# Optimization experiments

Hardware: AMD Instinct MI355X
Metric: run time of the kernel (lower is better)

Reference implementation:

```python
import jax, jax.numpy as jnp
import numpy as np

NUM_HEADS = 16


def setup_inputs() -> dict:
    key = jax.random.key(0)
    ks = jax.random.split(key, 5)
    B, L, D = 2, 2048, 1024
    x = jax.random.normal(ks[0], (B, L, D), dtype=jnp.float32)
    s = 1.0 / np.sqrt(D)
    Wqkv_w = jax.random.normal(ks[1], (3 * D, D), dtype=jnp.float32) * s
    Wqkv_b = jax.random.normal(ks[2], (3 * D,), dtype=jnp.float32) * 0.01
    out_w = jax.random.normal(ks[3], (D, D), dtype=jnp.float32) * s
    out_b = jax.random.normal(ks[4], (D,), dtype=jnp.float32) * 0.01
    return {"x": x, "Wqkv_w": Wqkv_w, "Wqkv_b": Wqkv_b, "out_w": out_w, "out_b": out_b}


def reference(x, Wqkv_w, Wqkv_b, out_w, out_b):
    B, L, D = x.shape
    H = NUM_HEADS
    d = D // H
    scale = 1.0 / np.sqrt(d).astype(np.float32)
    # qkv projection: torch Linear is x @ W^T + b
    qkv = x @ Wqkv_w.T + Wqkv_b                      # [B, L, 3D]
    qkv = qkv.reshape(B, L, 3, H, d)                 # (three h d) split
    qkv = jnp.transpose(qkv, (2, 0, 3, 1, 4))        # [3, B, H, L, d]
    q, k, v = qkv[0], qkv[1], qkv[2]
    k = k * scale
    # Linear-attention recurrence S_t = S_{t-1} + v_t k_t^T, y_t = S_t q_t
    # == causally-masked unnormalized attention: y_t = sum_{s<=t} (q_t.k_s) v_s
    scores = jnp.einsum('bhld,bhmd->bhlm', q, k)     # [B,H,L,L]
    causal = jnp.tril(jnp.ones((L, L), dtype=scores.dtype))
    y = jnp.einsum('bhlm,bhmd->bhld', scores * causal, v)  # [B,H,L,d]
    y = jnp.transpose(y, (0, 2, 1, 3)).reshape(B, L, D)    # b l (h d)
    return y @ out_w.T + out_b
```

## Files before the change

### kernel.cpp

```cpp
#include <hip/hip_runtime.h>


#define DEV __device__ __forceinline__

typedef __attribute__((ext_vector_type(8))) short bf16x8;
typedef __attribute__((ext_vector_type(4))) float f32x4;

DEV ushort f2bf(float f) {
  union { float f; unsigned u; } v; v.f = f;
  unsigned r = v.u + 0x7fffu + ((v.u >> 16) & 1u);
  return (ushort)(r >> 16);
}
DEV float bf2f(unsigned b) {
  union { unsigned u; float f; } v; v.u = (b & 0xffffu) << 16;
  return v.f;
}
DEV void glds16(const ushort* g, ushort* l) {
  __builtin_amdgcn_global_load_lds(
      (const __attribute__((address_space(1))) unsigned int*)g,
      (__attribute__((address_space(3))) unsigned int*)l, 16, 0, 0);
}

__global__ __launch_bounds__(256) void cvt_all(const float* __restrict__ x,
                                               const float* __restrict__ Ww,
                                               const float* __restrict__ Ow,
                                               ushort* __restrict__ xb,
                                               ushort* __restrict__ wqkvb,
                                               ushort* __restrict__ outwb) {
  int i = blockIdx.x * 256 + threadIdx.x;
  const float* src; ushort* dst; int off;
  if (i < 1048576)      { src = x;  dst = xb;    off = i; }
  else if (i < 1835008) { src = Ww; dst = wqkvb; off = i - 1048576; }
  else                  { src = Ow; dst = outwb; off = i - 1835008; }
  float4 v = ((const float4*)src)[off];
  ushort4 o;
  o.x = f2bf(v.x); o.y = f2bf(v.y); o.z = f2bf(v.z); o.w = f2bf(v.w);
  ((ushort4*)dst)[off] = o;
}

template <bool OUT_BF16, bool KSCALE>
__global__ __launch_bounds__(256) void gemm_bt(const ushort* __restrict__ A,
                                               const ushort* __restrict__ Bw,
                                               const float* __restrict__ bias,
                                               void* __restrict__ Cout,
                                               int M, int N, int K) {
  __shared__ ushort As[128 * 32];
  __shared__ ushort Bs[128 * 32];
  const int t = threadIdx.x;
  const int wid = t >> 6, lane = t & 63;
  const int quad = lane >> 4, l16 = lane & 15;
  const int bm = blockIdx.y * 128, bn = blockIdx.x * 128;
  const int wm = (wid >> 1) * 64, wn = (wid & 1) * 64;

  f32x4 acc[4][4];
  const f32x4 z = {0.f, 0.f, 0.f, 0.f};
#pragma unroll
  for (int i = 0; i < 4; ++i)
#pragma unroll
    for (int j = 0; j < 4; ++j) acc[i][j] = z;

  const ushort* ag = A + (size_t)(bm + (t >> 2)) * K + ((t & 3) * 8);
  const ushort* bg = Bw + (size_t)(bn + (t >> 2)) * K + ((t & 3) * 8);
  ushort* asl = As + wid * 512;
  ushort* bsl = Bs + wid * 512;
  const size_t rowskip = (size_t)64 * K;

  for (int k0 = 0; k0 < K; k0 += 32) {
    glds16(ag + k0, asl);
    glds16(ag + k0 + rowskip, asl + 2048);
    glds16(bg + k0, bsl);
    glds16(bg + k0 + rowskip, bsl + 2048);
    __syncthreads();
    bf16x8 af[4], bf[4];
#pragma unroll
    for (int i = 0; i < 4; ++i) {
      af[i] = *(const bf16x8*)(As + (wm + i * 16 + l16) * 32 + quad * 8);
      bf[i] = *(const bf16x8*)(Bs + (wn + i * 16 + l16) * 32 + quad * 8);
    }
#pragma unroll
    for (int i = 0; i < 4; ++i)
#pragma unroll
      for (int j = 0; j < 4; ++j)
        acc[i][j] = __builtin_amdgcn_mfma_f32_16x16x32_bf16(af[i], bf[j], acc[i][j], 0, 0, 0);
    __syncthreads();
  }

#pragma unroll
  for (int i = 0; i < 4; ++i)
#pragma unroll
    for (int j = 0; j < 4; ++j) {
      const int col = bn + wn + j * 16 + l16;
      const float bv = bias[col];
      float sc = 1.f;
      if (KSCALE) sc = ((col >> 10) == 1) ? 0.125f : 1.f;
#pragma unroll
      for (int r = 0; r < 4; ++r) {
        const int row = bm + wm + i * 16 + quad * 4 + r;
        const float v = (acc[i][j][r] + bv) * sc;
        if (OUT_BF16)
          ((ushort*)Cout)[(size_t)row * N + col] = f2bf(v);
        else
          ((float*)Cout)[(size_t)row * N + col] = v;
      }
    }
}

__global__ __launch_bounds__(256) void gemm_out64(const ushort* __restrict__ A,
                                                  const ushort* __restrict__ Bw,
                                                  const float* __restrict__ bias,
                                                  float* __restrict__ C,
                                                  int M, int N, int K) {
  __shared__ ushort As[64 * 32];
  __shared__ ushort Bs[128 * 32];
  const int t = threadIdx.x;
  const int wid = t >> 6, lane = t & 63;
  const int quad = lane >> 4, l16 = lane & 15;
  const int bm = blockIdx.y * 64, bn = blockIdx.x * 128;
  const int wn = wid * 32;

  f32x4 acc[4][2];
  const f32x4 z = {0.f, 0.f, 0.f, 0.f};
#pragma unroll
  for (int i = 0; i < 4; ++i) { acc[i][0] = z; acc[i][1] = z; }

  const ushort* ag = A + (size_t)(bm + (t >> 2)) * K + ((t & 3) * 8);
  const ushort* bg = Bw + (size_t)(bn + (t >> 2)) * K + ((t & 3) * 8);
  ushort* asl = As + wid * 512;
  ushort* bsl = Bs + wid * 512;
  const size_t rowskip = (size_t)64 * K;

  for (int k0 = 0; k0 < K; k0 += 32) {
    glds16(ag + k0, asl);
    glds16(bg + k0, bsl);
    glds16(bg + k0 + rowskip, bsl + 2048);
    __syncthreads();
    bf16x8 af[4], bf[2];
#pragma unroll
    for (int i = 0; i < 4; ++i)
      af[i] = *(const bf16x8*)(As + (i * 16 + l16) * 32 + quad * 8);
#pragma unroll
    for (int j = 0; j < 2; ++j)
      bf[j] = *(const bf16x8*)(Bs + (wn + j * 16 + l16) * 32 + quad * 8);
#pragma unroll
    for (int i = 0; i < 4; ++i)
#pragma unroll
      for (int j = 0; j < 2; ++j)
        acc[i][j] = __builtin_amdgcn_mfma_f32_16x16x32_bf16(af[i], bf[j], acc[i][j], 0, 0, 0);
    __syncthreads();
  }

#pragma unroll
  for (int i = 0; i < 4; ++i)
#pragma unroll
    for (int j = 0; j < 2; ++j) {
      const int col = bn + wn + j * 16 + l16;
      const float bv = bias[col];
#pragma unroll
      for (int r = 0; r < 4; ++r) {
        const int row = bm + i * 16 + quad * 4 + r;
        C[(size_t)row * N + col] = acc[i][j][r] + bv;
      }
    }
}

__global__ __launch_bounds__(256) void kv_local(const ushort* __restrict__ qkv,
                                                float* __restrict__ mlocT) {
  const int c = blockIdx.x, bh = blockIdx.y;
  const int b = bh >> 4, hd = bh & 15;
  const int t = threadIdx.x;
  const int wid = t >> 6, lane = t & 63;
  const int quad = lane >> 4, l16 = lane & 15;
  __shared__ ushort kT[64 * 136];
  __shared__ ushort vT[64 * 136];

  {
    const int row = t & 127;
    const int isv = t >> 7;
    const ushort* g = qkv + (size_t)(b * 2048 + c * 128 + row) * 3072 +
                      1024 + isv * 1024 + hd * 64;
    ushort tmp[64];
#pragma unroll
    for (int q = 0; q < 8; ++q) *(uint4*)(tmp + q * 8) = *(const uint4*)(g + q * 8);
    ushort* dst = isv ? vT : kT;
#pragma unroll
    for (int j = 0; j < 64; ++j) dst[j * 136 + row] = tmp[j];
  }
  __syncthreads();

  const f32x4 z = {0.f, 0.f, 0.f, 0.f};
  f32x4 acc[4];
#pragma unroll
  for (int ct = 0; ct < 4; ++ct) acc[ct] = z;
#pragma unroll
  for (int kc = 0; kc < 4; ++kc) {
    bf16x8 afr = *(const bf16x8*)(vT + (wid * 16 + l16) * 136 + kc * 32 + quad * 8);
#pragma unroll
    for (int ct = 0; ct < 4; ++ct) {
      bf16x8 bfr = *(const bf16x8*)(kT + (ct * 16 + l16) * 136 + kc * 32 + quad * 8);
      acc[ct] = __builtin_amdgcn_mfma_f32_16x16x32_bf16(afr, bfr, acc[ct], 0, 0, 0);
    }
  }

  float* outp = mlocT + ((size_t)bh * 16 + c) * 4096;
#pragma unroll
  for (int ct = 0; ct < 4; ++ct)
#pragma unroll
    for (int r = 0; r < 4; ++r)
      outp[(wid * 16 + quad * 4 + r) * 64 + ct * 16 + l16] = acc[ct][r];
}

__global__ __launch_bounds__(256) void attn_chunk(const ushort* __restrict__ qkv,
                                                  const float* __restrict__ mlocT,
                                                  ushort* __restrict__ yb) {
  const int c = blockIdx.x, bh = blockIdx.y;
  const int b = bh >> 4, hd = bh & 15;
  const int l0 = c * 128;
  const int t = threadIdx.x;
  const int wid = t >> 6, lane = t & 63;
  const int quad = lane >> 4, l16 = lane & 15;

  __shared__ ushort P[16384];
  __shared__ ushort U[16384];
  ushort* Qs = U;
  ushort* Ks = U + 8192;
  ushort* vT = U;
  ushort* sT = U + 8704;

  {
    uint4 zz; zz.x = zz.y = zz.z = zz.w = 0u;
    uint4* p4 = (uint4*)P;
#pragma unroll
    for (int i = 0; i < 8; ++i) p4[i * 256 + t] = zz;
  }
  {
    const int kcs = ((lane & 7) ^ (lane >> 3)) * 8;
    const ushort* qg = qkv + (size_t)(b * 2048 + l0 + (t >> 3)) * 3072 + hd * 64 + kcs;
    ushort* ql = Qs + wid * 512;
    ushort* kl = Ks + wid * 512;
#pragma unroll
    for (int h2 = 0; h2 < 4; ++h2) {
      glds16(qg + (size_t)h2 * 32 * 3072, ql + h2 * 2048);
      glds16(qg + (size_t)h2 * 32 * 3072 + 1024, kl + h2 * 2048);
    }
  }

  float run[16];
#pragma unroll
  for (int j = 0; j < 16; ++j) run[j] = 0.f;
  {
    const float4* mb = (const float4*)mlocT + (size_t)bh * 16384 + (size_t)t * 4;
    for (int cp = 0; cp < c; ++cp) {
      const float4* mc = mb + (size_t)cp * 1024;
#pragma unroll
      for (int k = 0; k < 4; ++k) {
        const float4 m = mc[k];
        run[k * 4 + 0] += m.x; run[k * 4 + 1] += m.y;
        run[k * 4 + 2] += m.z; run[k * 4 + 3] += m.w;
      }
    }
  }
  __syncthreads();

  bf16x8 qf[2][2];
#pragma unroll
  for (int i = 0; i < 2; ++i)
#pragma unroll
    for (int kc = 0; kc < 2; ++kc)
      qf[i][kc] = *(const bf16x8*)(Qs + ((wid * 2 + i) * 16 + l16) * 64 +
                                   (((kc * 4 + quad) ^ (l16 & 7)) * 8));

  const f32x4 z4 = {0.f, 0.f, 0.f, 0.f};
  f32x4 pacc[2][8];
#pragma unroll
  for (int i = 0; i < 2; ++i)
#pragma unroll
    for (int j = 0; j < 8; ++j) pacc[i][j] = z4;

#pragma unroll
  for (int i = 0; i < 2; ++i) {
    const int rt = wid * 2 + i;
#pragma unroll
    for (int tj = 0; tj < 8; ++tj) {
      if (tj <= rt) {
#pragma unroll
        for (int kc = 0; kc < 2; ++kc) {
          bf16x8 kfr = *(const bf16x8*)(Ks + (tj * 16 + l16) * 64 +
                                        (((kc * 4 + quad) ^ (l16 & 7)) * 8));
          pacc[i][tj] = __builtin_amdgcn_mfma_f32_16x16x32_bf16(qf[i][kc], kfr, pacc[i][tj], 0, 0, 0);
        }
      }
    }
  }
  __syncthreads();

#pragma unroll
  for (int i = 0; i < 2; ++i) {
    const int rt = wid * 2 + i;
#pragma unroll
    for (int tj = 0; tj < 8; ++tj) {
      if (tj <= rt) {
#pragma unroll
        for (int r = 0; r < 4; ++r) {
          const int row = rt * 16 + quad * 4 + r;
          const int scol = tj * 16 + l16;
          const float v = (scol <= row) ? pacc[i][tj][r] : 0.f;
          P[row * 128 + (((scol >> 3) ^ (row & 7)) * 8) + (scol & 7)] = f2bf(v);
        }
      }
    }
  }
  {
    const int sstep = t >> 1, eb = (t & 1) * 32;
    const ushort* vg = qkv + (size_t)(b * 2048 + l0 + sstep) * 3072 + 2048 + hd * 64 + eb;
    ushort tmp[32];
    *(uint4*)(tmp + 0)  = *(const uint4*)(vg + 0);
    *(uint4*)(tmp + 8)  = *(const uint4*)(vg + 8);
    *(uint4*)(tmp + 16) = *(const uint4*)(vg + 16);
    *(uint4*)(tmp + 24) = *(const uint4*)(vg + 24);
#pragma unroll
    for (int j = 0; j < 32; ++j) vT[(eb + j) * 136 + sstep] = tmp[j];
  }
  {
#pragma unroll
    for (int j = 0; j < 16; ++j) {
      const int ef = t * 16 + j;
      sT[(ef >> 6) * 72 + (ef & 63)] = f2bf(run[j]);
    }
  }
  __syncthreads();

  f32x4 yacc[2][4];
#pragma unroll
  for (int i = 0; i < 2; ++i)
#pragma unroll
    for (int j = 0; j < 4; ++j) yacc[i][j] = z4;

#pragma unroll
  for (int i = 0; i < 2; ++i) {
    const int rt = wid * 2 + i;
    const int kcmax = rt >> 1;
#pragma unroll
    for (int kc = 0; kc < 4; ++kc) {
      if (kc <= kcmax) {
        const int prow = rt * 16 + l16;
        bf16x8 pf;
        *(uint4*)&pf = *(const uint4*)(P + prow * 128 + (((kc * 4 + quad) ^ (prow & 7)) * 8));
#pragma unroll
        for (int ct = 0; ct < 4; ++ct) {
          bf16x8 vf = *(const bf16x8*)(vT + (ct * 16 + l16) * 136 + kc * 32 + quad * 8);
          yacc[i][ct] = __builtin_amdgcn_mfma_f32_16x16x32_bf16(pf, vf, yacc[i][ct], 0, 0, 0);
        }
      }
    }
#pragma unroll
    for (int kc = 0; kc < 2; ++kc) {
#pragma unroll
      for (int ct = 0; ct < 4; ++ct) {
        bf16x8 sf = *(const bf16x8*)(sT + (ct * 16 + l16) * 72 + kc * 32 + quad * 8);
        yacc[i][ct] = __builtin_amdgcn_mfma_f32_16x16x32_bf16(qf[i][kc], sf, yacc[i][ct], 0, 0, 0);
      }
    }
  }

#pragma unroll
  for (int i = 0; i < 2; ++i) {
    const int rt = wid * 2 + i;
#pragma unroll
    for (int ct = 0; ct < 4; ++ct) {
#pragma unroll
      for (int r = 0; r < 4; ++r) {
        const int row = rt * 16 + quad * 4 + r;
        const int e = ct * 16 + l16;
        yb[(size_t)(b * 2048 + l0 + row) * 1024 + hd * 64 + e] = f2bf(yacc[i][ct][r]);
      }
    }
  }
}

extern "C" void kernel_launch(void* const* d_in, const int* in_sizes, int n_in,
                              void* d_out, int out_size, void* d_ws, size_t ws_size,
                              hipStream_t stream) {
  const float* x  = (const float*)d_in[0];
  const float* Ww = (const float*)d_in[1];
  const float* Wb = (const float*)d_in[2];
  const float* Ow = (const float*)d_in[3];
  const float* Ob = (const float*)d_in[4];
  float* out = (float*)d_out;

  char* ws = (char*)d_ws;
  ushort* xb    = (ushort*)(ws);
  ushort* wqkvb = (ushort*)(ws + (size_t)8  * 1024 * 1024);
  ushort* outwb = (ushort*)(ws + (size_t)14 * 1024 * 1024);
  ushort* qkvb  = (ushort*)(ws + (size_t)16 * 1024 * 1024);
  float*  mlocT = (float*) (ws + (size_t)40 * 1024 * 1024);
  ushort* yb    = (ushort*)(ws + (size_t)48 * 1024 * 1024);

  cvt_all<<<8192, 256, 0, stream>>>(x, Ww, Ow, xb, wqkvb, outwb);
  gemm_bt<true, true><<<dim3(24, 32), 256, 0, stream>>>(xb, wqkvb, Wb, (void*)qkvb, 4096, 3072, 1024);
  kv_local<<<dim3(16, 32), 256, 0, stream>>>(qkvb, mlocT);
  attn_chunk<<<dim3(16, 32), 256, 0, stream>>>(qkvb, mlocT, yb);
  gemm_out64<<<dim3(8, 64), 256, 0, stream>>>(yb, outwb, Ob, out, 4096, 1024, 1024);
}
```

Measured before the change: 170.4 us.

## Deepen GEMM K-tile to 64 with XOR swizzle and add chunk-state prefix kernel

Both projection GEMMs now stage a 64-wide K slice per iteration, with an XOR-swizzled shared-memory layout. This halves the number of barrier round-trips and avoids bank conflicts on the fragment reads. A new kv_prefix kernel computes the exclusive prefix sum of per-chunk KV states once and stores it as bf16. attn_chunk then loads its state directly instead of having every block re-sum all earlier chunks, which removes redundant quadratic global reads. The cost is an extra kernel launch, doubled LDS per GEMM block, and a small bf16 rounding difference in the cumulative state.

```diff
diff --git a/kernel.cpp b/kernel.cpp
--- a/kernel.cpp
+++ b/kernel.cpp
@@ -44,11 +44,12 @@
                                                const float* __restrict__ bias,
                                                void* __restrict__ Cout,
                                                int M, int N, int K) {
-  __shared__ ushort As[128 * 32];
-  __shared__ ushort Bs[128 * 32];
+  __shared__ ushort As[128 * 64];
+  __shared__ ushort Bs[128 * 64];
   const int t = threadIdx.x;
   const int wid = t >> 6, lane = t & 63;
   const int quad = lane >> 4, l16 = lane & 15;
+  const int l3 = lane >> 3, l7 = lane & 7;
   const int bm = blockIdx.y * 128, bn = blockIdx.x * 128;
   const int wm = (wid >> 1) * 64, wn = (wid & 1) * 64;
 
@@ -59,29 +60,34 @@
 #pragma unroll
     for (int j = 0; j < 4; ++j) acc[i][j] = z;
 
-  const ushort* ag = A + (size_t)(bm + (t >> 2)) * K + ((t & 3) * 8);
-  const ushort* bg = Bw + (size_t)(bn + (t >> 2)) * K + ((t & 3) * 8);
+  const ushort* ag = A + (size_t)(bm + wid * 8 + l3) * K + ((l7 ^ (l3 & 7)) * 8);
+  const ushort* bg = Bw + (size_t)(bn + wid * 8 + l3) * K + ((l7 ^ (l3 & 7)) * 8);
   ushort* asl = As + wid * 512;
   ushort* bsl = Bs + wid * 512;
-  const size_t rowskip = (size_t)64 * K;
-
-  for (int k0 = 0; k0 < K; k0 += 32) {
-    glds16(ag + k0, asl);
-    glds16(ag + k0 + rowskip, asl + 2048);
-    glds16(bg + k0, bsl);
-    glds16(bg + k0 + rowskip, bsl + 2048);
+  const size_t rs = (size_t)32 * K;
+
+  for (int k0 = 0; k0 < K; k0 += 64) {
+#pragma unroll
+    for (int i = 0; i < 4; ++i) {
+      glds16(ag + k0 + (size_t)i * rs, asl + i * 2048);
+      glds16(bg + k0 + (size_t)i * rs, bsl + i * 2048);
+    }
     __syncthreads();
-    bf16x8 af[4], bf[4];
-#pragma unroll
-    for (int i = 0; i < 4; ++i) {
-      af[i] = *(const bf16x8*)(As + (wm + i * 16 + l16) * 32 + quad * 8);
-      bf[i] = *(const bf16x8*)(Bs + (wn + i * 16 + l16) * 32 + quad * 8);
-    }
-#pragma unroll
-    for (int i = 0; i < 4; ++i)
-#pragma unroll
-      for (int j = 0; j < 4; ++j)
-        acc[i][j] = __builtin_amdgcn_mfma_f32_16x16x32_bf16(af[i], bf[j], acc[i][j], 0, 0, 0);
+#pragma unroll
+    for (int ks = 0; ks < 2; ++ks) {
+      bf16x8 af[4], bf[4];
+#pragma unroll
+      for (int i = 0; i < 4; ++i) {
+        const int sw = (((ks * 4 + quad) ^ (l16 & 7)) * 8);
+        af[i] = *(const bf16x8*)(As + (wm + i * 16 + l16) * 64 + sw);
+        bf[i] = *(const bf16x8*)(Bs + (wn + i * 16 + l16) * 64 + sw);
+      }
+#pragma unroll
+      for (int i = 0; i < 4; ++i)
+#pragma unroll
+        for (int j = 0; j < 4; ++j)
+          acc[i][j] = __builtin_amdgcn_mfma_f32_16x16x32_bf16(af[i], bf[j], acc[i][j], 0, 0, 0);
+    }
     __syncthreads();
   }
 
@@ -110,11 +116,12 @@
                                                   const float* __restrict__ bias,
                                                   float* __restrict__ C,
                                                   int M, int N, int K) {
-  __shared__ ushort As[64 * 32];
-  __shared__ ushort Bs[128 * 32];
+  __shared__ ushort As[64 * 64];
+  __shared__ ushort Bs[128 * 64];
   const int t = threadIdx.x;
   const int wid = t >> 6, lane = t & 63;
   const int quad = lane >> 4, l16 = lane & 15;
+  const int l3 = lane >> 3, l7 = lane & 7;
   const int bm = blockIdx.y * 64, bn = blockIdx.x * 128;
   const int wn = wid * 32;
 
@@ -123,29 +130,34 @@
 #pragma unroll
   for (int i = 0; i < 4; ++i) { acc[i][0] = z; acc[i][1] = z; }
 
-  const ushort* ag = A + (size_t)(bm + (t >> 2)) * K + ((t & 3) * 8);
-  const ushort* bg = Bw + (size_t)(bn + (t >> 2)) * K + ((t & 3) * 8);
+  const ushort* ag = A + (size_t)(bm + wid * 8 + l3) * K + ((l7 ^ (l3 & 7)) * 8);
+  const ushort* bg = Bw + (size_t)(bn + wid * 8 + l3) * K + ((l7 ^ (l3 & 7)) * 8);
   ushort* asl = As + wid * 512;
   ushort* bsl = Bs + wid * 512;
-  const size_t rowskip = (size_t)64 * K;
-
-  for (int k0 = 0; k0 < K; k0 += 32) {
-    glds16(ag + k0, asl);
-    glds16(bg + k0, bsl);
-    glds16(bg + k0 + rowskip, bsl + 2048);
+  const size_t rs = (size_t)32 * K;
+
+  for (int k0 = 0; k0 < K; k0 += 64) {
+#pragma unroll
+    for (int i = 0; i < 2; ++i) glds16(ag + k0 + (size_t)i * rs, asl + i * 2048);
+#pragma unroll
+    for (int i = 0; i < 4; ++i) glds16(bg + k0 + (size_t)i * rs, bsl + i * 2048);
     __syncthreads();
-    bf16x8 af[4], bf[2];
-#pragma unroll
-    for (int i = 0; i < 4; ++i)
-      af[i] = *(const bf16x8*)(As + (i * 16 + l16) * 32 + quad * 8);
-#pragma unroll
-    for (int j = 0; j < 2; ++j)
-      bf[j] = *(const bf16x8*)(Bs + (wn + j * 16 + l16) * 32 + quad * 8);
-#pragma unroll
-    for (int i = 0; i < 4; ++i)
+#pragma unroll
+    for (int ks = 0; ks < 2; ++ks) {
+      const int sw = (((ks * 4 + quad) ^ (l16 & 7)) * 8);
+      bf16x8 af[4], bf[2];
+#pragma unroll
+      for (int i = 0; i < 4; ++i)
+        af[i] = *(const bf16x8*)(As + (i * 16 + l16) * 64 + sw);
 #pragma unroll
       for (int j = 0; j < 2; ++j)
-        acc[i][j] = __builtin_amdgcn_mfma_f32_16x16x32_bf16(af[i], bf[j], acc[i][j], 0, 0, 0);
+        bf[j] = *(const bf16x8*)(Bs + (wn + j * 16 + l16) * 64 + sw);
+#pragma unroll
+      for (int i = 0; i < 4; ++i)
+#pragma unroll
+        for (int j = 0; j < 2; ++j)
+          acc[i][j] = __builtin_amdgcn_mfma_f32_16x16x32_bf16(af[i], bf[j], acc[i][j], 0, 0, 0);
+    }
     __syncthreads();
   }
 
@@ -209,8 +221,20 @@
       outp[(wid * 16 + quad * 4 + r) * 64 + ct * 16 + l16] = acc[ct][r];
 }
 
+__global__ __launch_bounds__(256) void kv_prefix(const float* __restrict__ mlocT,
+                                                 ushort* __restrict__ statesT) {
+  const int slice = blockIdx.x, bh = blockIdx.y;
+  const int eidx = slice * 256 + threadIdx.x;
+  float run = 0.f;
+  for (int c = 0; c < 16; ++c) {
+    const size_t idx = ((size_t)bh * 16 + c) * 4096 + eidx;
+    statesT[idx] = f2bf(run);
+    run += mlocT[idx];
+  }
+}
+
 __global__ __launch_bounds__(256) void attn_chunk(const ushort* __restrict__ qkv,
-                                                  const float* __restrict__ mlocT,
+                                                  const ushort* __restrict__ statesT,
                                                   ushort* __restrict__ yb) {
   const int c = blockIdx.x, bh = blockIdx.y;
   const int b = bh >> 4, hd = bh & 15;
@@ -241,22 +265,6 @@
     for (int h2 = 0; h2 < 4; ++h2) {
       glds16(qg + (size_t)h2 * 32 * 3072, ql + h2 * 2048);
       glds16(qg + (size_t)h2 * 32 * 3072 + 1024, kl + h2 * 2048);
-    }
-  }
-
-  float run[16];
-#pragma unroll
-  for (int j = 0; j < 16; ++j) run[j] = 0.f;
-  {
-    const float4* mb = (const float4*)mlocT + (size_t)bh * 16384 + (size_t)t * 4;
-    for (int cp = 0; cp < c; ++cp) {
-      const float4* mc = mb + (size_t)cp * 1024;
-#pragma unroll
-      for (int k = 0; k < 4; ++k) {
-        const float4 m = mc[k];
-        run[k * 4 + 0] += m.x; run[k * 4 + 1] += m.y;
-        run[k * 4 + 2] += m.z; run[k * 4 + 3] += m.w;
-      }
     }
   }
   __syncthreads();
@@ -321,10 +329,12 @@
     for (int j = 0; j < 32; ++j) vT[(eb + j) * 136 + sstep] = tmp[j];
   }
   {
-#pragma unroll
-    for (int j = 0; j < 16; ++j) {
-      const int ef = t * 16 + j;
-      sT[(ef >> 6) * 72 + (ef & 63)] = f2bf(run[j]);
+    const ushort* sg = statesT + ((size_t)bh * 16 + c) * 4096;
+#pragma unroll
+    for (int h = 0; h < 2; ++h) {
+      const int cc = h * 256 + t;
+      uint4 d = *(const uint4*)(sg + cc * 8);
+      *(uint4*)(sT + (cc >> 3) * 72 + (cc & 7) * 8) = d;
     }
   }
   __syncthreads();
@@ -388,16 +398,18 @@
   float* out = (float*)d_out;
 
   char* ws = (char*)d_ws;
-  ushort* xb    = (ushort*)(ws);
-  ushort* wqkvb = (ushort*)(ws + (size_t)8  * 1024 * 1024);
-  ushort* outwb = (ushort*)(ws + (size_t)14 * 1024 * 1024);
-  ushort* qkvb  = (ushort*)(ws + (size_t)16 * 1024 * 1024);
-  float*  mlocT = (float*) (ws + (size_t)40 * 1024 * 1024);
-  ushort* yb    = (ushort*)(ws + (size_t)48 * 1024 * 1024);
+  ushort* xb      = (ushort*)(ws);
+  ushort* wqkvb   = (ushort*)(ws + (size_t)8  * 1024 * 1024);
+  ushort* outwb   = (ushort*)(ws + (size_t)14 * 1024 * 1024);
+  ushort* qkvb    = (ushort*)(ws + (size_t)16 * 1024 * 1024);
+  float*  mlocT   = (float*) (ws + (size_t)40 * 1024 * 1024);
+  ushort* statesT = (ushort*)(ws + (size_t)48 * 1024 * 1024);
+  ushort* yb      = (ushort*)(ws + (size_t)52 * 1024 * 1024);
 
   cvt_all<<<8192, 256, 0, stream>>>(x, Ww, Ow, xb, wqkvb, outwb);
   gemm_bt<true, true><<<dim3(24, 32), 256, 0, stream>>>(xb, wqkvb, Wb, (void*)qkvb, 4096, 3072, 1024);
   kv_local<<<dim3(16, 32), 256, 0, stream>>>(qkvb, mlocT);
-  attn_chunk<<<dim3(16, 32), 256, 0, stream>>>(qkvb, mlocT, yb);
+  kv_prefix<<<dim3(16, 32), 256, 0, stream>>>(mlocT, statesT);
+  attn_chunk<<<dim3(16, 32), 256, 0, stream>>>(qkvb, statesT, yb);
   gemm_out64<<<dim3(8, 64), 256, 0, stream>>>(yb, outwb, Ob, out, 4096, 1024, 1024);
 }
```

After: 164.7 us. 1.03x faster.

## Compute chunk state prefix sums in a separate kernel instead of per-block

Applied to the files above, without the earlier changes.

Adds a kv_prefix kernel that computes an exclusive prefix sum over the per-chunk KV states once and stores them as bf16. attn_chunk then loads its precomputed state with vector loads, instead of each block re-reading and summing all preceding chunk matrices. Without this, later chunks read up to 15 fp32 matrices, which is redundant global traffic and creates load imbalance across blocks. The cost is one extra kernel launch plus an extra write and read of the states buffer.

```diff
diff --git a/kernel.cpp b/kernel.cpp
--- a/kernel.cpp
+++ b/kernel.cpp
@@ -209,8 +209,20 @@
       outp[(wid * 16 + quad * 4 + r) * 64 + ct * 16 + l16] = acc[ct][r];
 }
 
+__global__ __launch_bounds__(256) void kv_prefix(const float* __restrict__ mlocT,
+                                                 ushort* __restrict__ statesT) {
+  const int slice = blockIdx.x, bh = blockIdx.y;
+  const int eidx = slice * 256 + threadIdx.x;
+  float run = 0.f;
+  for (int c = 0; c < 16; ++c) {
+    const size_t idx = ((size_t)bh * 16 + c) * 4096 + eidx;
+    statesT[idx] = f2bf(run);
+    run += mlocT[idx];
+  }
+}
+
 __global__ __launch_bounds__(256) void attn_chunk(const ushort* __restrict__ qkv,
-                                                  const float* __restrict__ mlocT,
+                                                  const ushort* __restrict__ statesT,
                                                   ushort* __restrict__ yb) {
   const int c = blockIdx.x, bh = blockIdx.y;
   const int b = bh >> 4, hd = bh & 15;
@@ -241,22 +253,6 @@
     for (int h2 = 0; h2 < 4; ++h2) {
       glds16(qg + (size_t)h2 * 32 * 3072, ql + h2 * 2048);
       glds16(qg + (size_t)h2 * 32 * 3072 + 1024, kl + h2 * 2048);
-    }
-  }
-
-  float run[16];
-#pragma unroll
-  for (int j = 0; j < 16; ++j) run[j] = 0.f;
-  {
-    const float4* mb = (const float4*)mlocT + (size_t)bh * 16384 + (size_t)t * 4;
-    for (int cp = 0; cp < c; ++cp) {
-      const float4* mc = mb + (size_t)cp * 1024;
-#pragma unroll
-      for (int k = 0; k < 4; ++k) {
-        const float4 m = mc[k];
-        run[k * 4 + 0] += m.x; run[k * 4 + 1] += m.y;
-        run[k * 4 + 2] += m.z; run[k * 4 + 3] += m.w;
-      }
     }
   }
   __syncthreads();
@@ -321,10 +317,12 @@
     for (int j = 0; j < 32; ++j) vT[(eb + j) * 136 + sstep] = tmp[j];
   }
   {
-#pragma unroll
-    for (int j = 0; j < 16; ++j) {
-      const int ef = t * 16 + j;
-      sT[(ef >> 6) * 72 + (ef & 63)] = f2bf(run[j]);
+    const ushort* sg = statesT + ((size_t)bh * 16 + c) * 4096;
+#pragma unroll
+    for (int h = 0; h < 2; ++h) {
+      const int cc = h * 256 + t;
+      uint4 d = *(const uint4*)(sg + cc * 8);
+      *(uint4*)(sT + (cc >> 3) * 72 + (cc & 7) * 8) = d;
     }
   }
   __syncthreads();
@@ -388,16 +386,18 @@
   float* out = (float*)d_out;
 
   char* ws = (char*)d_ws;
-  ushort* xb    = (ushort*)(ws);
-  ushort* wqkvb = (ushort*)(ws + (size_t)8  * 1024 * 1024);
-  ushort* outwb = (ushort*)(ws + (size_t)14 * 1024 * 1024);
-  ushort* qkvb  = (ushort*)(ws + (size_t)16 * 1024 * 1024);
-  float*  mlocT = (float*) (ws + (size_t)40 * 1024 * 1024);
-  ushort* yb    = (ushort*)(ws + (size_t)48 * 1024 * 1024);
+  ushort* xb      = (ushort*)(ws);
+  ushort* wqkvb   = (ushort*)(ws + (size_t)8  * 1024 * 1024);
+  ushort* outwb   = (ushort*)(ws + (size_t)14 * 1024 * 1024);
+  ushort* qkvb    = (ushort*)(ws + (size_t)16 * 1024 * 1024);
+  float*  mlocT   = (float*) (ws + (size_t)40 * 1024 * 1024);
+  ushort* statesT = (ushort*)(ws + (size_t)48 * 1024 * 1024);
+  ushort* yb      = (ushort*)(ws + (size_t)52 * 1024 * 1024);
 
   cvt_all<<<8192, 256, 0, stream>>>(x, Ww, Ow, xb, wqkvb, outwb);
   gemm_bt<true, true><<<dim3(24, 32), 256, 0, stream>>>(xb, wqkvb, Wb, (void*)qkvb, 4096, 3072, 1024);
   kv_local<<<dim3(16, 32), 256, 0, stream>>>(qkvb, mlocT);
-  attn_chunk<<<dim3(16, 32), 256, 0, stream>>>(qkvb, mlocT, yb);
+  kv_prefix<<<dim3(16, 32), 256, 0, stream>>>(mlocT, statesT);
+  attn_chunk<<<dim3(16, 32), 256, 0, stream>>>(qkvb, statesT, yb);
   gemm_out64<<<dim3(8, 64), 256, 0, stream>>>(yb, outwb, Ob, out, 4096, 1024, 1024);
 }
```

Measured after the change: 161.7 us. -5.1%, faster.
